# Kernel optimization log

Measured on AMD Instinct MI355X. Metric: run time of the kernel, lower is better.

## Reference

```python
import jax, jax.numpy as jnp
import numpy as np
import math


def _packet_loss_to_partial_patch(x, loss_rate):
    # Zero out randomly-chosen 1472-byte chunks of the NHWC-flattened tensor,
    # exactly mirroring the torch loop but as one vectorized masked multiply.
    B, C, H, W = x.shape
    xp = jnp.transpose(x, (0, 2, 3, 1)).reshape(-1)  # NHWC flatten
    n = xp.shape[0]
    elem_size = 4  # float32 bytes
    elems_per_chunk = 1472 // elem_size  # 368
    num_chunks = math.ceil(n * elem_size / 1472)
    num_lossy = int(math.ceil(num_chunks * (loss_rate / 100)))
    perm = jax.random.permutation(jax.random.key(1234), num_chunks)
    keep = jnp.ones((num_chunks,), xp.dtype).at[perm[:num_lossy]].set(0.0)
    elem_keep = jnp.repeat(keep, elems_per_chunk)[:n]
    xp = xp * elem_keep
    return jnp.transpose(xp.reshape(B, H, W, C), (0, 3, 1, 2))


def setup_inputs() -> dict:
    key = jax.random.key(0)
    ks = jax.random.split(key, 7)
    B, C, H, W = 32, 256, 56, 56
    r = 16
    s = 0.05
    return {
        "x": jax.random.normal(ks[0], (B, C, H, W), jnp.float32),
        "fc1_w": jax.random.normal(ks[1], (C // r, C), jnp.float32) * s,
        "fc2_w": jax.random.normal(ks[2], (C, C // r), jnp.float32) * s,
        "threshold": jnp.array([0.5], jnp.float32),
        "detect_w": jax.random.normal(ks[3], (C, C), jnp.float32) * s,
        "rec1_w": jax.random.normal(ks[4], (C, 2 * C), jnp.float32) * s,
        "rec2_w": jax.random.normal(ks[5], (C, C), jnp.float32) * s,
        "adapt_w": jax.random.normal(ks[6], (C, 1), jnp.float32) * s,
        "Packet_Loss_Rate": 50,
    }


def reference(x, fc1_w, fc2_w, threshold, detect_w, rec1_w, rec2_w, adapt_w, Packet_Loss_Rate):
    x = _packet_loss_to_partial_patch(x, Packet_Loss_Rate)
    B, C, H, W = x.shape
    # SE channel attention
    y = jnp.mean(x, axis=(2, 3))                              # [B, C]
    scores = jax.nn.sigmoid(jax.nn.relu(y @ fc1_w.T) @ fc2_w.T)  # [B, C]
    # packet-loss adaptation: Linear(1 -> C) applied to rate*ones([B,1])
    adapt = jnp.asarray(Packet_Loss_Rate, x.dtype) * adapt_w[:, 0]  # [C]
    mask = jax.nn.relu(scores + adapt[None, :] - threshold)   # [B, C]
    mask = mask[:, :, None, None]
    # 1x1 convs as channel GEMMs
    det = jnp.einsum('oc,bchw->bohw', detect_w, x)
    z = jnp.concatenate([x, jax.nn.sigmoid(det) * x], axis=1)  # [B, 2C, H, W]
    r = jax.nn.relu(jnp.einsum('oc,bchw->bohw', rec1_w, z))
    r = jnp.einsum('oc,bchw->bohw', rec2_w, r)
    return r * mask
```

## Files before the change

kernel.cpp:

```cpp
#include <hip/hip_runtime.h>
#include <stdint.h>

#define PARTITIONABLE 1

typedef float f32x4 __attribute__((ext_vector_type(4)));
typedef short bf16x8 __attribute__((ext_vector_type(8)));

namespace {
constexpr int Hh = 56, Ww = 56;
constexpr int HW = Hh * Ww;
constexpr int Bsz = 32, Cch = 256;
constexpr int NCH = 69811;
constexpr int HALF = 34906;
constexpr int NB2 = 4096;

constexpr int SC1_W   = 0;
constexpr int SC2_W   = 139648;
constexpr int BITS1_W = 279296;
constexpr int BITS2_W = 349120;
constexpr int R1_W    = 418944;
constexpr int R2_W    = 488768;
constexpr int HIST1_W = 558592;
constexpr int PRE1_W  = 562688;
constexpr int CNT1_W  = 566784;
constexpr int HIST2_W = 570880;
constexpr int PRE2_W  = 574976;
constexpr int CNT2_W  = 579072;
constexpr int Y_W     = 583168;

constexpr int KEEP_W  = 0;
constexpr int MASKV_W = 69824;
constexpr int WPACK_W = 78016;
}

__host__ __device__ constexpr uint32_t rotl32(uint32_t v, int r) {
  return (v << r) | (v >> (32 - r));
}
__host__ __device__ constexpr uint64_t tf2x32(uint32_t k0, uint32_t k1,
                                              uint32_t x0, uint32_t x1) {
  uint32_t ks2 = k0 ^ k1 ^ 0x1BD11BDAu;
  x0 += k0; x1 += k1;
  {const int R[4]={13,15,26,6};  for(int i=0;i<4;i++){x0+=x1;x1=rotl32(x1,R[i]);x1^=x0;}}
  x0 += k1;  x1 += ks2 + 1u;
  {const int R[4]={17,29,16,24}; for(int i=0;i<4;i++){x0+=x1;x1=rotl32(x1,R[i]);x1^=x0;}}
  x0 += ks2; x1 += k0 + 2u;
  {const int R[4]={13,15,26,6};  for(int i=0;i<4;i++){x0+=x1;x1=rotl32(x1,R[i]);x1^=x0;}}
  x0 += k0;  x1 += k1 + 3u;
  {const int R[4]={17,29,16,24}; for(int i=0;i<4;i++){x0+=x1;x1=rotl32(x1,R[i]);x1^=x0;}}
  x0 += k1;  x1 += ks2 + 4u;
  {const int R[4]={13,15,26,6};  for(int i=0;i<4;i++){x0+=x1;x1=rotl32(x1,R[i]);x1^=x0;}}
  x0 += ks2; x1 += k0 + 5u;
  return ((uint64_t)x0 << 32) | x1;
}

#if PARTITIONABLE
constexpr uint64_t KEY1 = tf2x32(0u, 1234u, 0u, 0u);
constexpr uint64_t SUB1 = tf2x32(0u, 1234u, 0u, 1u);
constexpr uint64_t SUB2 = tf2x32((uint32_t)(KEY1 >> 32), (uint32_t)KEY1, 0u, 1u);
constexpr uint32_t S1H = (uint32_t)(SUB1 >> 32), S1L = (uint32_t)SUB1;
constexpr uint32_t S2H = (uint32_t)(SUB2 >> 32), S2L = (uint32_t)SUB2;
#else
constexpr uint64_t E0 = tf2x32(0u, 1234u, 0u, 2u);
constexpr uint64_t E1 = tf2x32(0u, 1234u, 1u, 3u);
constexpr uint32_t K1H = (uint32_t)(E0 >> 32), K1L = (uint32_t)(E1 >> 32);
constexpr uint64_t F0 = tf2x32(K1H, K1L, 0u, 2u);
constexpr uint64_t F1 = tf2x32(K1H, K1L, 1u, 3u);
constexpr uint32_t S1H = (uint32_t)E0, S1L = (uint32_t)E1;
constexpr uint32_t S2H = (uint32_t)F0, S2L = (uint32_t)F1;
#endif

__device__ __forceinline__ uint32_t rnd_bits(uint32_t kh, uint32_t kl, uint32_t i) {
#if PARTITIONABLE
  uint64_t r = tf2x32(kh, kl, 0u, i);
  return (uint32_t)(r >> 32) ^ (uint32_t)r;
#else
  if (i < (uint32_t)HALF) {
    uint32_t x1 = (i + HALF < (uint32_t)NCH) ? i + HALF : 0u;
    return (uint32_t)(tf2x32(kh, kl, i, x1) >> 32);
  } else {
    return (uint32_t)tf2x32(kh, kl, i - HALF, i);
  }
#endif
}

__device__ __forceinline__ uint32_t f2bf(float f) {
  uint32_t u = __float_as_uint(f);
  return (u + 0x7FFFu + ((u >> 16) & 1u)) >> 16;
}
__device__ __forceinline__ float bf2f(uint32_t h) {
  return __uint_as_float(h << 16);
}

__global__ void k_bits(uint32_t* bits1, uint32_t* bits2,
                       uint32_t* hist1, uint32_t* hist2) {
  int i = blockIdx.x * 256 + threadIdx.x;
  if (i >= NCH) return;
  uint32_t b1 = rnd_bits(S1H, S1L, (uint32_t)i);
  uint32_t b2 = rnd_bits(S2H, S2L, (uint32_t)i);
  bits1[i] = b1; bits2[i] = b2;
  atomicAdd(&hist1[b1 >> 20], 1u);
  atomicAdd(&hist2[b2 >> 20], 1u);
}

__global__ __launch_bounds__(1024) void k_scan2(const uint32_t* h1, uint32_t* p1o,
                                                const uint32_t* h2, uint32_t* p2o) {
  const uint32_t* h = blockIdx.x ? h2 : h1;
  uint32_t* pre = blockIdx.x ? p2o : p1o;
  __shared__ uint32_t part[1024];
  int t = threadIdx.x;
  uint4 v = *(const uint4*)&h[t * 4];
  uint32_t s = v.x + v.y + v.z + v.w;
  part[t] = s;
  __syncthreads();
  for (int off = 1; off < 1024; off <<= 1) {
    uint32_t u = (t >= off) ? part[t - off] : 0u;
    __syncthreads();
    part[t] += u;
    __syncthreads();
  }
  uint32_t run = part[t] - s;
  uint4 o;
  o.x = run; o.y = run + v.x; o.z = o.y + v.y; o.w = o.z + v.z;
  *(uint4*)&pre[t * 4] = o;
}

__global__ void k_scatter2(const uint32_t* bits1, const uint32_t* pre1,
                           uint32_t* cnt1, uint64_t* sc1,
                           const uint32_t* bits2, const uint32_t* pre2,
                           uint32_t* cnt2, uint64_t* sc2) {
  int blk = blockIdx.x;
  bool second = blk >= 273;
  const uint32_t* bits = second ? bits2 : bits1;
  const uint32_t* pre  = second ? pre2  : pre1;
  uint32_t* cnt = second ? cnt2 : cnt1;
  uint64_t* sc  = second ? sc2  : sc1;
  int i = (second ? blk - 273 : blk) * 256 + threadIdx.x;
  if (i >= NCH) return;
  uint32_t b = bits[i], bk = b >> 20;
  uint32_t pos = pre[bk] + atomicAdd(&cnt[bk], 1u);
  sc[pos] = ((uint64_t)b << 32) | (uint32_t)i;
}

__global__ void k_rank2(const uint32_t* bits1, const uint32_t* pre1,
                        const uint32_t* hist1, const uint64_t* sc1, uint32_t* rk1,
                        const uint32_t* bits2, const uint32_t* pre2,
                        const uint32_t* hist2, const uint64_t* sc2, uint32_t* rk2) {
  int blk = blockIdx.x;
  bool second = blk >= 273;
  const uint32_t* bits = second ? bits2 : bits1;
  const uint32_t* pre  = second ? pre2  : pre1;
  const uint32_t* hist = second ? hist2 : hist1;
  const uint64_t* sc   = second ? sc2   : sc1;
  uint32_t* rnk = second ? rk2 : rk1;
  int i = (second ? blk - 273 : blk) * 256 + threadIdx.x;
  if (i >= NCH) return;
  uint32_t b = bits[i], bk = b >> 20;
  uint32_t s = pre[bk], n = hist[bk];
  uint64_t my = ((uint64_t)b << 32) | (uint32_t)i;
  uint32_t c = 0;
  for (uint32_t k = 0; k < n; ++k) c += (sc[s + k] < my) ? 1u : 0u;
  rnk[i] = s + c;
}

__global__ void k_keepwpack(const uint32_t* r1, const uint32_t* r2,
                            const int* plr, float* keep,
                            const float* __restrict__ dw,
                            const float* __restrict__ r1w,
                            const float* __restrict__ r2w,
                            ushort* __restrict__ wdp, ushort* __restrict__ w1p,
                            ushort* __restrict__ w2p) {
  int blk = blockIdx.x;
  if (blk < 273) {
    int j = blk * 256 + threadIdx.x;
    if (j >= NCH) return;
    int L = (NCH * plr[0] + 99) / 100;
    keep[j] = (r2[r1[j]] < (uint32_t)L) ? 0.f : 1.f;
    return;
  }
  int tid = (blk - 273) * 256 + threadIdx.x;
  const float* src;
  ushort* dst;
  if (tid < 8192) {
    int s = tid, ot = s >> 9, ks = (s >> 6) & 7, l = s & 63;
    src = dw + (ot * 16 + (l & 15)) * 256 + ks * 32 + (l >> 4) * 8;
    dst = wdp + s * 8;
  } else if (tid < 24576) {
    int s = tid - 8192, ot = s >> 10, ks = (s >> 6) & 15, l = s & 63;
    src = r1w + (ot * 16 + (l & 15)) * 512 + ks * 32 + (l >> 4) * 8;
    dst = w1p + s * 8;
  } else {
    int s = tid - 24576, ot = s >> 9, ks = (s >> 6) & 7, l = s & 63;
    src = r2w + (ot * 16 + (l & 15)) * 256 + ks * 32 + (l >> 4) * 8;
    dst = w2p + s * 8;
  }
  float4 v0 = *(const float4*)src;
  float4 v1 = *(const float4*)(src + 4);
  uint4 pk;
  pk.x = f2bf(v0.x) | (f2bf(v0.y) << 16);
  pk.y = f2bf(v0.z) | (f2bf(v0.w) << 16);
  pk.z = f2bf(v1.x) | (f2bf(v1.y) << 16);
  pk.w = f2bf(v1.z) | (f2bf(v1.w) << 16);
  *(uint4*)dst = pk;
}

__global__ void k_ymean(const float* __restrict__ x, const float* __restrict__ keep,
                        float* __restrict__ y) {
  int bc = blockIdx.x;
  int b = bc >> 8, c = bc & 255;
  const float4* row = (const float4*)(x + (size_t)bc * HW);
  int t = threadIdx.x;
  float s = 0.f;
  for (int q = t; q < HW / 4; q += 256) {
    float4 v = row[q];
    uint32_t base = (uint32_t)((b * HW + q * 4) * 256 + c);
    s += v.x * keep[base / 368u];
    s += v.y * keep[(base + 256u) / 368u];
    s += v.z * keep[(base + 512u) / 368u];
    s += v.w * keep[(base + 768u) / 368u];
  }
  for (int off = 32; off > 0; off >>= 1) s += __shfl_down(s, off);
  __shared__ float w4[4];
  if ((t & 63) == 0) w4[t >> 6] = s;
  __syncthreads();
  if (t == 0) y[bc] = (w4[0] + w4[1] + w4[2] + w4[3]) * (1.0f / HW);
}

__global__ void k_scores(const float* __restrict__ y, const float* __restrict__ fc1,
                         const float* __restrict__ fc2, const float* __restrict__ thr,
                         const float* __restrict__ aw, const int* __restrict__ plr,
                         float* __restrict__ maskv) {
  int b = blockIdx.x, t = threadIdx.x;
  __shared__ float ysh[256];
  __shared__ float hsh[16];
  ysh[t] = y[b * 256 + t];
  __syncthreads();
  if (t < 16) {
    float a = 0.f;
    for (int c = 0; c < 256; ++c) a += ysh[c] * fc1[t * 256 + c];
    hsh[t] = fmaxf(a, 0.f);
  }
  __syncthreads();
  float s = 0.f;
  #pragma unroll
  for (int j = 0; j < 16; ++j) s += hsh[j] * fc2[t * 16 + j];
  float sc = 1.f / (1.f + expf(-s));
  float m = sc + (float)plr[0] * aw[t] - thr[0];
  maskv[b * 256 + t] = fmaxf(m, 0.f);
}

__global__ __launch_bounds__(512, 4) void k_main(
    const float* __restrict__ x, const float* __restrict__ keep,
    const ushort* __restrict__ wdp, const ushort* __restrict__ w1p,
    const ushort* __restrict__ w2p, const float* __restrict__ maskv,
    float* __restrict__ out) {
  __shared__ __align__(16) short XT[16384];
  __shared__ __align__(16) short ST[16384];
  int tile = blockIdx.x;
  int bb = tile / 49, hw0 = (tile % 49) * 64;
  int t = threadIdx.x;
  int lane = t & 63, w = t >> 6;
  int l15 = lane & 15, lhi = lane >> 4;

  {
    const float* xb = x + (size_t)bb * (Cch * HW);
    uint32_t pixb = (uint32_t)(bb * HW + hw0);
    int p = lane;
    uint32_t ia0 = (pixb + (uint32_t)p) * 256u;
    uint32_t k0 = ia0 / 368u;
    uint32_t cstar = 368u * (k0 + 1u) - ia0;
    float kp0 = keep[k0];
    float kp1 = keep[k0 + 1];
    const float* xcol = xb + hw0 + p;
    int c0 = w * 32;
    #pragma unroll
    for (int k = 0; k < 4; ++k) {
      uint32_t pw0, pw1, pw2, pw3;
      #pragma unroll
      for (int h = 0; h < 4; ++h) {
        uint32_t ca = (uint32_t)(c0 + k * 8 + h * 2);
        float va = xcol[(size_t)ca * HW] * (ca < cstar ? kp0 : kp1);
        float vb = xcol[(size_t)(ca + 1u) * HW] * ((ca + 1u) < cstar ? kp0 : kp1);
        uint32_t pkv = f2bf(va) | (f2bf(vb) << 16);
        if (h == 0) pw0 = pkv; else if (h == 1) pw1 = pkv;
        else if (h == 2) pw2 = pkv; else pw3 = pkv;
      }
      uint4 pk; pk.x = pw0; pk.y = pw1; pk.z = pw2; pk.w = pw3;
      *(uint4*)&XT[(w * 4 + (p >> 4)) * 512 + ((p & 15) + 16 * k) * 8] = pk;
    }
  }
  __syncthreads();

  f32x4 zero4 = {0.f, 0.f, 0.f, 0.f};
  f32x4 acc[2][4];
  int row16a = (lhi >> 1);
  int sub4 = (lhi & 1) * 4;

  #pragma unroll
  for (int mt = 0; mt < 2; ++mt)
    #pragma unroll
    for (int nt = 0; nt < 4; ++nt) acc[mt][nt] = zero4;
  {
    const ushort* a0p = wdp + ((w * 2 + 0) * 8) * 512 + lane * 8;
    const ushort* a1p = wdp + ((w * 2 + 1) * 8) * 512 + lane * 8;
    bf16x8 a0 = *(const bf16x8*)a0p;
    bf16x8 a1 = *(const bf16x8*)a1p;
    #pragma unroll
    for (int ks = 0; ks < 8; ++ks) {
      bf16x8 na0 = a0, na1 = a1;
      if (ks < 7) {
        na0 = *(const bf16x8*)(a0p + (ks + 1) * 512);
        na1 = *(const bf16x8*)(a1p + (ks + 1) * 512);
      }
      #pragma unroll
      for (int nt = 0; nt < 4; ++nt) {
        bf16x8 b = *(const bf16x8*)&XT[(ks * 4 + nt) * 512 + lane * 8];
        acc[0][nt] = __builtin_amdgcn_mfma_f32_16x16x32_bf16(a0, b, acc[0][nt], 0, 0, 0);
        acc[1][nt] = __builtin_amdgcn_mfma_f32_16x16x32_bf16(a1, b, acc[1][nt], 0, 0, 0);
      }
      a0 = na0; a1 = na1;
    }
  }

  #pragma unroll
  for (int mt = 0; mt < 2; ++mt) {
    int row16 = mt * 2 + row16a;
    #pragma unroll
    for (int nt = 0; nt < 4; ++nt) {
      int off = (w * 4 + nt) * 512 + (l15 + 16 * row16) * 8 + sub4;
      ushort4 xv = *(const ushort4*)&XT[off];
      ushort4 sv;
      sv.x = (ushort)f2bf(bf2f(xv.x) / (1.f + __expf(-acc[mt][nt][0])));
      sv.y = (ushort)f2bf(bf2f(xv.y) / (1.f + __expf(-acc[mt][nt][1])));
      sv.z = (ushort)f2bf(bf2f(xv.z) / (1.f + __expf(-acc[mt][nt][2])));
      sv.w = (ushort)f2bf(bf2f(xv.w) / (1.f + __expf(-acc[mt][nt][3])));
      *(ushort4*)&ST[off] = sv;
    }
  }
  __syncthreads();

  f32x4 acc2[2][4];
  #pragma unroll
  for (int mt = 0; mt < 2; ++mt)
    #pragma unroll
    for (int nt = 0; nt < 4; ++nt) acc2[mt][nt] = zero4;
  {
    const ushort* a0p = w1p + ((w * 2 + 0) * 16) * 512 + lane * 8;
    const ushort* a1p = w1p + ((w * 2 + 1) * 16) * 512 + lane * 8;
    bf16x8 a0 = *(const bf16x8*)a0p;
    bf16x8 a1 = *(const bf16x8*)a1p;
    #pragma unroll
    for (int ks = 0; ks < 16; ++ks) {
      bf16x8 na0 = a0, na1 = a1;
      if (ks < 15) {
        na0 = *(const bf16x8*)(a0p + (ks + 1) * 512);
        na1 = *(const bf16x8*)(a1p + (ks + 1) * 512);
      }
      const short* bsrc = (ks < 8) ? &XT[(ks * 4) * 512] : &ST[((ks - 8) * 4) * 512];
      #pragma unroll
      for (int nt = 0; nt < 4; ++nt) {
        bf16x8 b = *(const bf16x8*)&bsrc[nt * 512 + lane * 8];
        acc2[0][nt] = __builtin_amdgcn_mfma_f32_16x16x32_bf16(a0, b, acc2[0][nt], 0, 0, 0);
        acc2[1][nt] = __builtin_amdgcn_mfma_f32_16x16x32_bf16(a1, b, acc2[1][nt], 0, 0, 0);
      }
      a0 = na0; a1 = na1;
    }
  }
  __syncthreads();

  #pragma unroll
  for (int mt = 0; mt < 2; ++mt) {
    int row16 = mt * 2 + row16a;
    #pragma unroll
    for (int nt = 0; nt < 4; ++nt) {
      int off = (w * 4 + nt) * 512 + (l15 + 16 * row16) * 8 + sub4;
      ushort4 rv;
      rv.x = (ushort)f2bf(fmaxf(acc2[mt][nt][0], 0.f));
      rv.y = (ushort)f2bf(fmaxf(acc2[mt][nt][1], 0.f));
      rv.z = (ushort)f2bf(fmaxf(acc2[mt][nt][2], 0.f));
      rv.w = (ushort)f2bf(fmaxf(acc2[mt][nt][3], 0.f));
      *(ushort4*)&XT[off] = rv;
    }
  }
  __syncthreads();

  #pragma unroll
  for (int mt = 0; mt < 2; ++mt)
    #pragma unroll
    for (int nt = 0; nt < 4; ++nt) acc[mt][nt] = zero4;
  {
    const ushort* a0p = w2p + ((w * 2 + 0) * 8) * 512 + lane * 8;
    const ushort* a1p = w2p + ((w * 2 + 1) * 8) * 512 + lane * 8;
    bf16x8 a0 = *(const bf16x8*)a0p;
    bf16x8 a1 = *(const bf16x8*)a1p;
    #pragma unroll
    for (int ks = 0; ks < 8; ++ks) {
      bf16x8 na0 = a0, na1 = a1;
      if (ks < 7) {
        na0 = *(const bf16x8*)(a0p + (ks + 1) * 512);
        na1 = *(const bf16x8*)(a1p + (ks + 1) * 512);
      }
      #pragma unroll
      for (int nt = 0; nt < 4; ++nt) {
        bf16x8 b = *(const bf16x8*)&XT[(ks * 4 + nt) * 512 + lane * 8];
        acc[0][nt] = __builtin_amdgcn_mfma_f32_16x16x32_bf16(a0, b, acc[0][nt], 0, 0, 0);
        acc[1][nt] = __builtin_amdgcn_mfma_f32_16x16x32_bf16(a1, b, acc[1][nt], 0, 0, 0);
      }
      a0 = na0; a1 = na1;
    }
  }

  #pragma unroll
  for (int mt = 0; mt < 2; ++mt)
    #pragma unroll
    for (int r = 0; r < 4; ++r) {
      int o = w * 32 + mt * 16 + 4 * lhi + r;
      float m = maskv[bb * 256 + o];
      float* orow = out + (size_t)(bb * 256 + o) * HW + hw0;
      #pragma unroll
      for (int nt = 0; nt < 4; ++nt)
        orow[nt * 16 + l15] = acc[mt][nt][r] * m;
    }
}

extern "C" void kernel_launch(void* const* d_in, const int* in_sizes, int n_in,
                              void* d_out, int out_size, void* d_ws, size_t ws_size,
                              hipStream_t stream) {
  const float* x   = (const float*)d_in[0];
  const float* fc1 = (const float*)d_in[1];
  const float* fc2 = (const float*)d_in[2];
  const float* thr = (const float*)d_in[3];
  const float* dw  = (const float*)d_in[4];
  const float* r1w = (const float*)d_in[5];
  const float* r2w = (const float*)d_in[6];
  const float* aw  = (const float*)d_in[7];
  const int*   plr = (const int*)d_in[8];

  float*    out = (float*)d_out;
  uint32_t* ob  = (uint32_t*)d_out;
  float*    ws  = (float*)d_ws;

  uint64_t* sc1   = (uint64_t*)(ob + SC1_W);
  uint64_t* sc2   = (uint64_t*)(ob + SC2_W);
  uint32_t* bits1 = ob + BITS1_W;
  uint32_t* bits2 = ob + BITS2_W;
  uint32_t* r1    = ob + R1_W;
  uint32_t* r2    = ob + R2_W;
  uint32_t* hist1 = ob + HIST1_W;
  uint32_t* pre1  = ob + PRE1_W;
  uint32_t* cnt1  = ob + CNT1_W;
  uint32_t* hist2 = ob + HIST2_W;
  uint32_t* pre2  = ob + PRE2_W;
  uint32_t* cnt2  = ob + CNT2_W;
  float*    yv    = (float*)(ob + Y_W);

  float*  keep  = ws + KEEP_W;
  float*  maskv = ws + MASKV_W;
  ushort* wdp   = (ushort*)(ws + WPACK_W);
  ushort* w1p   = wdp + 65536;
  ushort* w2p   = w1p + 131072;

  hipMemsetAsync((void*)(ob + HIST1_W), 0, (size_t)6 * NB2 * 4, stream);

  dim3 blk(256);
  k_bits<<<273, blk, 0, stream>>>(bits1, bits2, hist1, hist2);
  k_scan2<<<2, 1024, 0, stream>>>(hist1, pre1, hist2, pre2);
  k_scatter2<<<546, blk, 0, stream>>>(bits1, pre1, cnt1, sc1,
                                      bits2, pre2, cnt2, sc2);
  k_rank2<<<546, blk, 0, stream>>>(bits1, pre1, hist1, sc1, r1,
                                   bits2, pre2, hist2, sc2, r2);
  k_keepwpack<<<401, blk, 0, stream>>>(r1, r2, plr, keep, dw, r1w, r2w,
                                       wdp, w1p, w2p);
  k_ymean<<<8192, blk, 0, stream>>>(x, keep, yv);
  k_scores<<<32, blk, 0, stream>>>(yv, fc1, fc2, thr, aw, plr, maskv);
  k_main<<<1568, 512, 0, stream>>>(x, keep, wdp, w1p, w2p, maskv, out);
}
```

Baseline: 149.9 us.

## Split main kernel over 16 waves, use hardware bf16 pack, stage output in LDS

Measured after the change: 158.5 us. 5.8% more time.

```diff
diff --git a/kernel.cpp b/kernel.cpp
--- a/kernel.cpp
+++ b/kernel.cpp
@@ -89,6 +89,11 @@
 }
 __device__ __forceinline__ float bf2f(uint32_t h) {
   return __uint_as_float(h << 16);
+}
+__device__ __forceinline__ uint32_t cvtpk(float lo, float hi) {
+  uint32_t r;
+  asm("v_cvt_pk_bf16_f32 %0, %1, %2" : "=v"(r) : "v"(lo), "v"(hi));
+  return r;
 }
 
 __global__ void k_bits(uint32_t* bits1, uint32_t* bits2,
@@ -248,13 +253,12 @@
   maskv[b * 256 + t] = fmaxf(m, 0.f);
 }
 
-__global__ __launch_bounds__(512, 4) void k_main(
+__global__ __launch_bounds__(1024, 8) void k_main(
     const float* __restrict__ x, const float* __restrict__ keep,
     const ushort* __restrict__ wdp, const ushort* __restrict__ w1p,
     const ushort* __restrict__ w2p, const float* __restrict__ maskv,
     float* __restrict__ out) {
-  __shared__ __align__(16) short XT[16384];
-  __shared__ __align__(16) short ST[16384];
+  __shared__ __align__(16) short SM[32768];
   int tile = blockIdx.x;
   int bb = tile / 49, hw0 = (tile % 49) * 64;
   int t = threadIdx.x;
@@ -271,155 +275,138 @@
     float kp0 = keep[k0];
     float kp1 = keep[k0 + 1];
     const float* xcol = xb + hw0 + p;
-    int c0 = w * 32;
-    #pragma unroll
-    for (int k = 0; k < 4; ++k) {
-      uint32_t pw0, pw1, pw2, pw3;
+    int ks = w >> 1;
+    #pragma unroll
+    for (int k2 = 0; k2 < 2; ++k2) {
+      int k = (w & 1) * 2 + k2;
+      int cb = ks * 32 + k * 8;
+      uint32_t pw[4];
       #pragma unroll
       for (int h = 0; h < 4; ++h) {
-        uint32_t ca = (uint32_t)(c0 + k * 8 + h * 2);
+        uint32_t ca = (uint32_t)(cb + h * 2);
         float va = xcol[(size_t)ca * HW] * (ca < cstar ? kp0 : kp1);
         float vb = xcol[(size_t)(ca + 1u) * HW] * ((ca + 1u) < cstar ? kp0 : kp1);
-        uint32_t pkv = f2bf(va) | (f2bf(vb) << 16);
-        if (h == 0) pw0 = pkv; else if (h == 1) pw1 = pkv;
-        else if (h == 2) pw2 = pkv; else pw3 = pkv;
+        pw[h] = cvtpk(va, vb);
       }
-      uint4 pk; pk.x = pw0; pk.y = pw1; pk.z = pw2; pk.w = pw3;
-      *(uint4*)&XT[(w * 4 + (p >> 4)) * 512 + ((p & 15) + 16 * k) * 8] = pk;
+      uint4 pk; pk.x = pw[0]; pk.y = pw[1]; pk.z = pw[2]; pk.w = pw[3];
+      *(uint4*)&SM[(ks * 4 + (p >> 4)) * 512 + ((p & 15) + 16 * k) * 8] = pk;
     }
   }
   __syncthreads();
 
   f32x4 zero4 = {0.f, 0.f, 0.f, 0.f};
-  f32x4 acc[2][4];
-  int row16a = (lhi >> 1);
-  int sub4 = (lhi & 1) * 4;
-
-  #pragma unroll
-  for (int mt = 0; mt < 2; ++mt)
-    #pragma unroll
-    for (int nt = 0; nt < 4; ++nt) acc[mt][nt] = zero4;
-  {
-    const ushort* a0p = wdp + ((w * 2 + 0) * 8) * 512 + lane * 8;
-    const ushort* a1p = wdp + ((w * 2 + 1) * 8) * 512 + lane * 8;
-    bf16x8 a0 = *(const bf16x8*)a0p;
-    bf16x8 a1 = *(const bf16x8*)a1p;
+  f32x4 acc[4];
+  int stoff = ((w >> 1) * 4) * 512 +
+              (l15 + 16 * ((w & 1) * 2 + (lhi >> 1))) * 8 + (lhi & 1) * 4;
+
+  #pragma unroll
+  for (int nt = 0; nt < 4; ++nt) acc[nt] = zero4;
+  {
+    const ushort* ap = wdp + (w * 8) * 512 + lane * 8;
+    bf16x8 a0 = *(const bf16x8*)ap;
     #pragma unroll
     for (int ks = 0; ks < 8; ++ks) {
-      bf16x8 na0 = a0, na1 = a1;
-      if (ks < 7) {
-        na0 = *(const bf16x8*)(a0p + (ks + 1) * 512);
-        na1 = *(const bf16x8*)(a1p + (ks + 1) * 512);
-      }
+      bf16x8 na0 = a0;
+      if (ks < 7) na0 = *(const bf16x8*)(ap + (ks + 1) * 512);
       #pragma unroll
       for (int nt = 0; nt < 4; ++nt) {
-        bf16x8 b = *(const bf16x8*)&XT[(ks * 4 + nt) * 512 + lane * 8];
-        acc[0][nt] = __builtin_amdgcn_mfma_f32_16x16x32_bf16(a0, b, acc[0][nt], 0, 0, 0);
-        acc[1][nt] = __builtin_amdgcn_mfma_f32_16x16x32_bf16(a1, b, acc[1][nt], 0, 0, 0);
+        bf16x8 b = *(const bf16x8*)&SM[(ks * 4 + nt) * 512 + lane * 8];
+        acc[nt] = __builtin_amdgcn_mfma_f32_16x16x32_bf16(a0, b, acc[nt], 0, 0, 0);
       }
-      a0 = na0; a1 = na1;
-    }
-  }
-
-  #pragma unroll
-  for (int mt = 0; mt < 2; ++mt) {
-    int row16 = mt * 2 + row16a;
-    #pragma unroll
-    for (int nt = 0; nt < 4; ++nt) {
-      int off = (w * 4 + nt) * 512 + (l15 + 16 * row16) * 8 + sub4;
-      ushort4 xv = *(const ushort4*)&XT[off];
-      ushort4 sv;
-      sv.x = (ushort)f2bf(bf2f(xv.x) / (1.f + __expf(-acc[mt][nt][0])));
-      sv.y = (ushort)f2bf(bf2f(xv.y) / (1.f + __expf(-acc[mt][nt][1])));
-      sv.z = (ushort)f2bf(bf2f(xv.z) / (1.f + __expf(-acc[mt][nt][2])));
-      sv.w = (ushort)f2bf(bf2f(xv.w) / (1.f + __expf(-acc[mt][nt][3])));
-      *(ushort4*)&ST[off] = sv;
-    }
-  }
-  __syncthreads();
-
-  f32x4 acc2[2][4];
-  #pragma unroll
-  for (int mt = 0; mt < 2; ++mt)
-    #pragma unroll
-    for (int nt = 0; nt < 4; ++nt) acc2[mt][nt] = zero4;
-  {
-    const ushort* a0p = w1p + ((w * 2 + 0) * 16) * 512 + lane * 8;
-    const ushort* a1p = w1p + ((w * 2 + 1) * 16) * 512 + lane * 8;
-    bf16x8 a0 = *(const bf16x8*)a0p;
-    bf16x8 a1 = *(const bf16x8*)a1p;
+      a0 = na0;
+    }
+  }
+
+  #pragma unroll
+  for (int nt = 0; nt < 4; ++nt) {
+    int off = stoff + nt * 512;
+    ushort4 xv = *(const ushort4*)&SM[off];
+    float s0 = bf2f(xv.x) / (1.f + __expf(-acc[nt][0]));
+    float s1 = bf2f(xv.y) / (1.f + __expf(-acc[nt][1]));
+    float s2 = bf2f(xv.z) / (1.f + __expf(-acc[nt][2]));
+    float s3 = bf2f(xv.w) / (1.f + __expf(-acc[nt][3]));
+    uint2 sv;
+    sv.x = cvtpk(s0, s1);
+    sv.y = cvtpk(s2, s3);
+    *(uint2*)&SM[16384 + off] = sv;
+  }
+  __syncthreads();
+
+  f32x4 acc2[4];
+  #pragma unroll
+  for (int nt = 0; nt < 4; ++nt) acc2[nt] = zero4;
+  {
+    const ushort* ap = w1p + (w * 16) * 512 + lane * 8;
+    bf16x8 a0 = *(const bf16x8*)ap;
     #pragma unroll
     for (int ks = 0; ks < 16; ++ks) {
-      bf16x8 na0 = a0, na1 = a1;
-      if (ks < 15) {
-        na0 = *(const bf16x8*)(a0p + (ks + 1) * 512);
-        na1 = *(const bf16x8*)(a1p + (ks + 1) * 512);
-      }
-      const short* bsrc = (ks < 8) ? &XT[(ks * 4) * 512] : &ST[((ks - 8) * 4) * 512];
+      bf16x8 na0 = a0;
+      if (ks < 15) na0 = *(const bf16x8*)(ap + (ks + 1) * 512);
       #pragma unroll
       for (int nt = 0; nt < 4; ++nt) {
-        bf16x8 b = *(const bf16x8*)&bsrc[nt * 512 + lane * 8];
-        acc2[0][nt] = __builtin_amdgcn_mfma_f32_16x16x32_bf16(a0, b, acc2[0][nt], 0, 0, 0);
-        acc2[1][nt] = __builtin_amdgcn_mfma_f32_16x16x32_bf16(a1, b, acc2[1][nt], 0, 0, 0);
+        bf16x8 b = *(const bf16x8*)&SM[(ks * 4 + nt) * 512 + lane * 8];
+        acc2[nt] = __builtin_amdgcn_mfma_f32_16x16x32_bf16(a0, b, acc2[nt], 0, 0, 0);
       }
-      a0 = na0; a1 = na1;
-    }
-  }
-  __syncthreads();
-
-  #pragma unroll
-  for (int mt = 0; mt < 2; ++mt) {
-    int row16 = mt * 2 + row16a;
-    #pragma unroll
-    for (int nt = 0; nt < 4; ++nt) {
-      int off = (w * 4 + nt) * 512 + (l15 + 16 * row16) * 8 + sub4;
-      ushort4 rv;
-      rv.x = (ushort)f2bf(fmaxf(acc2[mt][nt][0], 0.f));
-      rv.y = (ushort)f2bf(fmaxf(acc2[mt][nt][1], 0.f));
-      rv.z = (ushort)f2bf(fmaxf(acc2[mt][nt][2], 0.f));
-      rv.w = (ushort)f2bf(fmaxf(acc2[mt][nt][3], 0.f));
-      *(ushort4*)&XT[off] = rv;
-    }
-  }
-  __syncthreads();
-
-  #pragma unroll
-  for (int mt = 0; mt < 2; ++mt)
-    #pragma unroll
-    for (int nt = 0; nt < 4; ++nt) acc[mt][nt] = zero4;
-  {
-    const ushort* a0p = w2p + ((w * 2 + 0) * 8) * 512 + lane * 8;
-    const ushort* a1p = w2p + ((w * 2 + 1) * 8) * 512 + lane * 8;
-    bf16x8 a0 = *(const bf16x8*)a0p;
-    bf16x8 a1 = *(const bf16x8*)a1p;
+      a0 = na0;
+    }
+  }
+  __syncthreads();
+
+  #pragma unroll
+  for (int nt = 0; nt < 4; ++nt) {
+    int off = stoff + nt * 512;
+    uint2 rv;
+    rv.x = cvtpk(fmaxf(acc2[nt][0], 0.f), fmaxf(acc2[nt][1], 0.f));
+    rv.y = cvtpk(fmaxf(acc2[nt][2], 0.f), fmaxf(acc2[nt][3], 0.f));
+    *(uint2*)&SM[off] = rv;
+  }
+  __syncthreads();
+
+  #pragma unroll
+  for (int nt = 0; nt < 4; ++nt) acc[nt] = zero4;
+  {
+    const ushort* ap = w2p + (w * 8) * 512 + lane * 8;
+    bf16x8 a0 = *(const bf16x8*)ap;
     #pragma unroll
     for (int ks = 0; ks < 8; ++ks) {
-      bf16x8 na0 = a0, na1 = a1;
-      if (ks < 7) {
-        na0 = *(const bf16x8*)(a0p + (ks + 1) * 512);
-        na1 = *(const bf16x8*)(a1p + (ks + 1) * 512);
-      }
+      bf16x8 na0 = a0;
+      if (ks < 7) na0 = *(const bf16x8*)(ap + (ks + 1) * 512);
       #pragma unroll
       for (int nt = 0; nt < 4; ++nt) {
-        bf16x8 b = *(const bf16x8*)&XT[(ks * 4 + nt) * 512 + lane * 8];
-        acc[0][nt] = __builtin_amdgcn_mfma_f32_16x16x32_bf16(a0, b, acc[0][nt], 0, 0, 0);
-        acc[1][nt] = __builtin_amdgcn_mfma_f32_16x16x32_bf16(a1, b, acc[1][nt], 0, 0, 0);
+        bf16x8 b = *(const bf16x8*)&SM[(ks * 4 + nt) * 512 + lane * 8];
+        acc[nt] = __builtin_amdgcn_mfma_f32_16x16x32_bf16(a0, b, acc[nt], 0, 0, 0);
       }
-      a0 = na0; a1 = na1;
-    }
-  }
-
-  #pragma unroll
-  for (int mt = 0; mt < 2; ++mt)
+      a0 = na0;
+    }
+  }
+  __syncthreads();
+
+  {
+    float* EP = (float*)SM;
+    int sw = ((lhi & 1) << 2) | ((lhi >> 1) << 4);
     #pragma unroll
     for (int r = 0; r < 4; ++r) {
-      int o = w * 32 + mt * 16 + 4 * lhi + r;
-      float m = maskv[bb * 256 + o];
-      float* orow = out + (size_t)(bb * 256 + o) * HW + hw0;
+      int c = w * 16 + 4 * lhi + r;
+      float m = maskv[bb * 256 + c];
       #pragma unroll
       for (int nt = 0; nt < 4; ++nt)
-        orow[nt * 16 + l15] = acc[mt][nt][r] * m;
-    }
+        EP[c * 64 + ((nt * 16 + l15) ^ sw)] = acc[nt][r] * m;
+    }
+  }
+  __syncthreads();
+  {
+    const float* EP = (const float*)SM;
+    float* op = out + (size_t)bb * (Cch * HW) + hw0;
+    #pragma unroll
+    for (int q = 0; q < 4; ++q) {
+      int idx4 = q * 1024 + t;
+      int c = idx4 >> 4;
+      int colw = (idx4 & 15) * 4;
+      int p = colw ^ ((((c >> 2) & 1) << 2) | (((c >> 3) & 1) << 4));
+      f32x4 v = *(const f32x4*)&EP[idx4 * 4];
+      *(f32x4*)(op + (size_t)c * HW + p) = v;
+    }
+  }
 }
 
 extern "C" void kernel_launch(void* const* d_in, const int* in_sizes, int n_in,
@@ -472,5 +459,5 @@
                                        wdp, w1p, w2p);
   k_ymean<<<8192, blk, 0, stream>>>(x, keep, yv);
   k_scores<<<32, blk, 0, stream>>>(yv, fc1, fc2, thr, aw, plr, maskv);
-  k_main<<<1568, 512, 0, stream>>>(x, keep, wdp, w1p, w2p, maskv, out);
-}
+  k_main<<<1568, 1024, 0, stream>>>(x, keep, wdp, w1p, w2p, maskv, out);
+}
```

## Retile k_main warps to 4x2 MFMA tiles, fuse ymean+scores, use packed bf16 cvt

Applied to the files above, without the earlier changes.

Measured after the change: 230.1 us. 53.6% more time.

```diff
diff --git a/kernel.cpp b/kernel.cpp
--- a/kernel.cpp
+++ b/kernel.cpp
@@ -26,7 +26,8 @@
 constexpr int HIST2_W = 570880;
 constexpr int PRE2_W  = 574976;
 constexpr int CNT2_W  = 579072;
-constexpr int Y_W     = 583168;
+constexpr int DONE_W  = 583168;
+constexpr int Y_W     = 583200;
 
 constexpr int KEEP_W  = 0;
 constexpr int MASKV_W = 69824;
@@ -89,6 +90,11 @@
 }
 __device__ __forceinline__ float bf2f(uint32_t h) {
   return __uint_as_float(h << 16);
+}
+__device__ __forceinline__ uint32_t cvtpk(float lo, float hi) {
+  uint32_t r;
+  asm("v_cvt_pk_bf16_f32 %0, %1, %2" : "=v"(r) : "v"(lo), "v"(hi));
+  return r;
 }
 
 __global__ void k_bits(uint32_t* bits1, uint32_t* bits2,
@@ -203,36 +209,45 @@
   *(uint4*)dst = pk;
 }
 
-__global__ void k_ymean(const float* __restrict__ x, const float* __restrict__ keep,
-                        float* __restrict__ y) {
-  int bc = blockIdx.x;
-  int b = bc >> 8, c = bc & 255;
-  const float4* row = (const float4*)(x + (size_t)bc * HW);
-  int t = threadIdx.x;
-  float s = 0.f;
-  for (int q = t; q < HW / 4; q += 256) {
-    float4 v = row[q];
-    uint32_t base = (uint32_t)((b * HW + q * 4) * 256 + c);
-    s += v.x * keep[base / 368u];
-    s += v.y * keep[(base + 256u) / 368u];
-    s += v.z * keep[(base + 512u) / 368u];
-    s += v.w * keep[(base + 768u) / 368u];
-  }
-  for (int off = 32; off > 0; off >>= 1) s += __shfl_down(s, off);
-  __shared__ float w4[4];
-  if ((t & 63) == 0) w4[t >> 6] = s;
-  __syncthreads();
-  if (t == 0) y[bc] = (w4[0] + w4[1] + w4[2] + w4[3]) * (1.0f / HW);
-}
-
-__global__ void k_scores(const float* __restrict__ y, const float* __restrict__ fc1,
-                         const float* __restrict__ fc2, const float* __restrict__ thr,
-                         const float* __restrict__ aw, const int* __restrict__ plr,
-                         float* __restrict__ maskv) {
-  int b = blockIdx.x, t = threadIdx.x;
+__global__ __launch_bounds__(256) void k_ymean2(
+    const float* __restrict__ x, const float* __restrict__ keep,
+    float* __restrict__ y, uint32_t* __restrict__ done,
+    const float* __restrict__ fc1, const float* __restrict__ fc2,
+    const float* __restrict__ thr, const float* __restrict__ aw,
+    const int* __restrict__ plr, float* __restrict__ maskv) {
+  int blk = blockIdx.x;
+  int b = blk >> 5, sub = blk & 31;
+  int t = threadIdx.x, lane = t & 63, v = t >> 6;
+  #pragma unroll
+  for (int cc = 0; cc < 2; ++cc) {
+    int c = sub * 8 + v * 2 + cc;
+    int row = b * 256 + c;
+    const float4* rowp = (const float4*)(x + (size_t)row * HW);
+    float s = 0.f;
+    for (int q = lane; q < HW / 4; q += 64) {
+      float4 vv = rowp[q];
+      uint32_t base = (uint32_t)((b * HW + q * 4) * 256 + c);
+      s += vv.x * keep[base / 368u];
+      s += vv.y * keep[(base + 256u) / 368u];
+      s += vv.z * keep[(base + 512u) / 368u];
+      s += vv.w * keep[(base + 768u) / 368u];
+    }
+    for (int off = 32; off > 0; off >>= 1) s += __shfl_down(s, off);
+    if (lane == 0) y[row] = s * (1.0f / HW);
+  }
+  __threadfence();
+  __syncthreads();
+  __shared__ int lastf;
+  if (t == 0) {
+    uint32_t ret = atomicAdd(&done[b], 1u);
+    lastf = (ret == 31u) ? 1 : 0;
+  }
+  __syncthreads();
+  if (!lastf) return;
+  __threadfence();
   __shared__ float ysh[256];
   __shared__ float hsh[16];
-  ysh[t] = y[b * 256 + t];
+  ysh[t] = ((volatile const float*)y)[b * 256 + t];
   __syncthreads();
   if (t < 16) {
     float a = 0.f;
@@ -260,6 +275,7 @@
   int t = threadIdx.x;
   int lane = t & 63, w = t >> 6;
   int l15 = lane & 15, lhi = lane >> 4;
+  int g = w >> 1, h = w & 1;
 
   {
     const float* xb = x + (size_t)bb * (Cch * HW);
@@ -276,13 +292,13 @@
     for (int k = 0; k < 4; ++k) {
       uint32_t pw0, pw1, pw2, pw3;
       #pragma unroll
-      for (int h = 0; h < 4; ++h) {
-        uint32_t ca = (uint32_t)(c0 + k * 8 + h * 2);
+      for (int hh = 0; hh < 4; ++hh) {
+        uint32_t ca = (uint32_t)(c0 + k * 8 + hh * 2);
         float va = xcol[(size_t)ca * HW] * (ca < cstar ? kp0 : kp1);
         float vb = xcol[(size_t)(ca + 1u) * HW] * ((ca + 1u) < cstar ? kp0 : kp1);
-        uint32_t pkv = f2bf(va) | (f2bf(vb) << 16);
-        if (h == 0) pw0 = pkv; else if (h == 1) pw1 = pkv;
-        else if (h == 2) pw2 = pkv; else pw3 = pkv;
+        uint32_t pkv = cvtpk(va, vb);
+        if (hh == 0) pw0 = pkv; else if (hh == 1) pw1 = pkv;
+        else if (hh == 2) pw2 = pkv; else pw3 = pkv;
       }
       uint4 pk; pk.x = pw0; pk.y = pw1; pk.z = pw2; pk.w = pw3;
       *(uint4*)&XT[(w * 4 + (p >> 4)) * 512 + ((p & 15) + 16 * k) * 8] = pk;
@@ -291,134 +307,138 @@
   __syncthreads();
 
   f32x4 zero4 = {0.f, 0.f, 0.f, 0.f};
-  f32x4 acc[2][4];
+  f32x4 acc[4][2];
   int row16a = (lhi >> 1);
   int sub4 = (lhi & 1) * 4;
 
   #pragma unroll
-  for (int mt = 0; mt < 2; ++mt)
-    #pragma unroll
-    for (int nt = 0; nt < 4; ++nt) acc[mt][nt] = zero4;
+  for (int mt = 0; mt < 4; ++mt)
+    #pragma unroll
+    for (int n2 = 0; n2 < 2; ++n2) acc[mt][n2] = zero4;
   {
-    const ushort* a0p = wdp + ((w * 2 + 0) * 8) * 512 + lane * 8;
-    const ushort* a1p = wdp + ((w * 2 + 1) * 8) * 512 + lane * 8;
-    bf16x8 a0 = *(const bf16x8*)a0p;
-    bf16x8 a1 = *(const bf16x8*)a1p;
+    const ushort* ap = wdp + (size_t)(g * 32) * 512 + lane * 8;
+    bf16x8 a[4], na[4];
+    #pragma unroll
+    for (int mt = 0; mt < 4; ++mt) a[mt] = *(const bf16x8*)(ap + (size_t)mt * 8 * 512);
     #pragma unroll
     for (int ks = 0; ks < 8; ++ks) {
-      bf16x8 na0 = a0, na1 = a1;
-      if (ks < 7) {
-        na0 = *(const bf16x8*)(a0p + (ks + 1) * 512);
-        na1 = *(const bf16x8*)(a1p + (ks + 1) * 512);
+      #pragma unroll
+      for (int mt = 0; mt < 4; ++mt)
+        na[mt] = (ks < 7) ? *(const bf16x8*)(ap + (size_t)(mt * 8 + ks + 1) * 512) : a[mt];
+      #pragma unroll
+      for (int n2 = 0; n2 < 2; ++n2) {
+        bf16x8 b = *(const bf16x8*)&XT[(ks * 4 + 2 * h + n2) * 512 + lane * 8];
+        #pragma unroll
+        for (int mt = 0; mt < 4; ++mt)
+          acc[mt][n2] = __builtin_amdgcn_mfma_f32_16x16x32_bf16(a[mt], b, acc[mt][n2], 0, 0, 0);
       }
       #pragma unroll
-      for (int nt = 0; nt < 4; ++nt) {
-        bf16x8 b = *(const bf16x8*)&XT[(ks * 4 + nt) * 512 + lane * 8];
-        acc[0][nt] = __builtin_amdgcn_mfma_f32_16x16x32_bf16(a0, b, acc[0][nt], 0, 0, 0);
-        acc[1][nt] = __builtin_amdgcn_mfma_f32_16x16x32_bf16(a1, b, acc[1][nt], 0, 0, 0);
+      for (int mt = 0; mt < 4; ++mt) a[mt] = na[mt];
+    }
+  }
+
+  #pragma unroll
+  for (int mt = 0; mt < 4; ++mt) {
+    int cg32 = 2 * g + (mt >> 1);
+    int row16 = (mt & 1) * 2 + row16a;
+    #pragma unroll
+    for (int n2 = 0; n2 < 2; ++n2) {
+      int nt = 2 * h + n2;
+      int off = (cg32 * 4 + nt) * 512 + (l15 + 16 * row16) * 8 + sub4;
+      ushort4 xv = *(const ushort4*)&XT[off];
+      float s0 = bf2f(xv.x) / (1.f + __expf(-acc[mt][n2][0]));
+      float s1 = bf2f(xv.y) / (1.f + __expf(-acc[mt][n2][1]));
+      float s2 = bf2f(xv.z) / (1.f + __expf(-acc[mt][n2][2]));
+      float s3 = bf2f(xv.w) / (1.f + __expf(-acc[mt][n2][3]));
+      uint2 sv;
+      sv.x = cvtpk(s0, s1);
+      sv.y = cvtpk(s2, s3);
+      *(uint2*)&ST[off] = sv;
+    }
+  }
+  __syncthreads();
+
+  f32x4 acc2[4][2];
+  #pragma unroll
+  for (int mt = 0; mt < 4; ++mt)
+    #pragma unroll
+    for (int n2 = 0; n2 < 2; ++n2) acc2[mt][n2] = zero4;
+  {
+    const ushort* ap = w1p + (size_t)(g * 64) * 512 + lane * 8;
+    bf16x8 a[4], na[4];
+    #pragma unroll
+    for (int mt = 0; mt < 4; ++mt) a[mt] = *(const bf16x8*)(ap + (size_t)mt * 16 * 512);
+    #pragma unroll
+    for (int ks = 0; ks < 16; ++ks) {
+      #pragma unroll
+      for (int mt = 0; mt < 4; ++mt)
+        na[mt] = (ks < 15) ? *(const bf16x8*)(ap + (size_t)(mt * 16 + ks + 1) * 512) : a[mt];
+      const short* bsrc = (ks < 8) ? &XT[(ks * 4) * 512] : &ST[((ks - 8) * 4) * 512];
+      #pragma unroll
+      for (int n2 = 0; n2 < 2; ++n2) {
+        bf16x8 b = *(const bf16x8*)&bsrc[(2 * h + n2) * 512 + lane * 8];
+        #pragma unroll
+        for (int mt = 0; mt < 4; ++mt)
+          acc2[mt][n2] = __builtin_amdgcn_mfma_f32_16x16x32_bf16(a[mt], b, acc2[mt][n2], 0, 0, 0);
       }
-      a0 = na0; a1 = na1;
-    }
-  }
-
-  #pragma unroll
-  for (int mt = 0; mt < 2; ++mt) {
-    int row16 = mt * 2 + row16a;
-    #pragma unroll
-    for (int nt = 0; nt < 4; ++nt) {
-      int off = (w * 4 + nt) * 512 + (l15 + 16 * row16) * 8 + sub4;
-      ushort4 xv = *(const ushort4*)&XT[off];
-      ushort4 sv;
-      sv.x = (ushort)f2bf(bf2f(xv.x) / (1.f + __expf(-acc[mt][nt][0])));
-      sv.y = (ushort)f2bf(bf2f(xv.y) / (1.f + __expf(-acc[mt][nt][1])));
-      sv.z = (ushort)f2bf(bf2f(xv.z) / (1.f + __expf(-acc[mt][nt][2])));
-      sv.w = (ushort)f2bf(bf2f(xv.w) / (1.f + __expf(-acc[mt][nt][3])));
-      *(ushort4*)&ST[off] = sv;
-    }
-  }
-  __syncthreads();
-
-  f32x4 acc2[2][4];
-  #pragma unroll
-  for (int mt = 0; mt < 2; ++mt)
-    #pragma unroll
-    for (int nt = 0; nt < 4; ++nt) acc2[mt][nt] = zero4;
+      #pragma unroll
+      for (int mt = 0; mt < 4; ++mt) a[mt] = na[mt];
+    }
+  }
+  __syncthreads();
+
+  #pragma unroll
+  for (int mt = 0; mt < 4; ++mt) {
+    int cg32 = 2 * g + (mt >> 1);
+    int row16 = (mt & 1) * 2 + row16a;
+    #pragma unroll
+    for (int n2 = 0; n2 < 2; ++n2) {
+      int nt = 2 * h + n2;
+      int off = (cg32 * 4 + nt) * 512 + (l15 + 16 * row16) * 8 + sub4;
+      uint2 rv;
+      rv.x = cvtpk(fmaxf(acc2[mt][n2][0], 0.f), fmaxf(acc2[mt][n2][1], 0.f));
+      rv.y = cvtpk(fmaxf(acc2[mt][n2][2], 0.f), fmaxf(acc2[mt][n2][3], 0.f));
+      *(uint2*)&XT[off] = rv;
+    }
+  }
+  __syncthreads();
+
+  #pragma unroll
+  for (int mt = 0; mt < 4; ++mt)
+    #pragma unroll
+    for (int n2 = 0; n2 < 2; ++n2) acc[mt][n2] = zero4;
   {
-    const ushort* a0p = w1p + ((w * 2 + 0) * 16) * 512 + lane * 8;
-    const ushort* a1p = w1p + ((w * 2 + 1) * 16) * 512 + lane * 8;
-    bf16x8 a0 = *(const bf16x8*)a0p;
-    bf16x8 a1 = *(const bf16x8*)a1p;
-    #pragma unroll
-    for (int ks = 0; ks < 16; ++ks) {
-      bf16x8 na0 = a0, na1 = a1;
-      if (ks < 15) {
-        na0 = *(const bf16x8*)(a0p + (ks + 1) * 512);
-        na1 = *(const bf16x8*)(a1p + (ks + 1) * 512);
+    const ushort* ap = w2p + (size_t)(g * 32) * 512 + lane * 8;
+    bf16x8 a[4], na[4];
+    #pragma unroll
+    for (int mt = 0; mt < 4; ++mt) a[mt] = *(const bf16x8*)(ap + (size_t)mt * 8 * 512);
+    #pragma unroll
+    for (int ks = 0; ks < 8; ++ks) {
+      #pragma unroll
+      for (int mt = 0; mt < 4; ++mt)
+        na[mt] = (ks < 7) ? *(const bf16x8*)(ap + (size_t)(mt * 8 + ks + 1) * 512) : a[mt];
+      #pragma unroll
+      for (int n2 = 0; n2 < 2; ++n2) {
+        bf16x8 b = *(const bf16x8*)&XT[(ks * 4 + 2 * h + n2) * 512 + lane * 8];
+        #pragma unroll
+        for (int mt = 0; mt < 4; ++mt)
+          acc[mt][n2] = __builtin_amdgcn_mfma_f32_16x16x32_bf16(a[mt], b, acc[mt][n2], 0, 0, 0);
       }
-      const short* bsrc = (ks < 8) ? &XT[(ks * 4) * 512] : &ST[((ks - 8) * 4) * 512];
-      #pragma unroll
-      for (int nt = 0; nt < 4; ++nt) {
-        bf16x8 b = *(const bf16x8*)&bsrc[nt * 512 + lane * 8];
-        acc2[0][nt] = __builtin_amdgcn_mfma_f32_16x16x32_bf16(a0, b, acc2[0][nt], 0, 0, 0);
-        acc2[1][nt] = __builtin_amdgcn_mfma_f32_16x16x32_bf16(a1, b, acc2[1][nt], 0, 0, 0);
-      }
-      a0 = na0; a1 = na1;
-    }
-  }
-  __syncthreads();
-
-  #pragma unroll
-  for (int mt = 0; mt < 2; ++mt) {
-    int row16 = mt * 2 + row16a;
-    #pragma unroll
-    for (int nt = 0; nt < 4; ++nt) {
-      int off = (w * 4 + nt) * 512 + (l15 + 16 * row16) * 8 + sub4;
-      ushort4 rv;
-      rv.x = (ushort)f2bf(fmaxf(acc2[mt][nt][0], 0.f));
-      rv.y = (ushort)f2bf(fmaxf(acc2[mt][nt][1], 0.f));
-      rv.z = (ushort)f2bf(fmaxf(acc2[mt][nt][2], 0.f));
-      rv.w = (ushort)f2bf(fmaxf(acc2[mt][nt][3], 0.f));
-      *(ushort4*)&XT[off] = rv;
-    }
-  }
-  __syncthreads();
-
-  #pragma unroll
-  for (int mt = 0; mt < 2; ++mt)
-    #pragma unroll
-    for (int nt = 0; nt < 4; ++nt) acc[mt][nt] = zero4;
-  {
-    const ushort* a0p = w2p + ((w * 2 + 0) * 8) * 512 + lane * 8;
-    const ushort* a1p = w2p + ((w * 2 + 1) * 8) * 512 + lane * 8;
-    bf16x8 a0 = *(const bf16x8*)a0p;
-    bf16x8 a1 = *(const bf16x8*)a1p;
-    #pragma unroll
-    for (int ks = 0; ks < 8; ++ks) {
-      bf16x8 na0 = a0, na1 = a1;
-      if (ks < 7) {
-        na0 = *(const bf16x8*)(a0p + (ks + 1) * 512);
-        na1 = *(const bf16x8*)(a1p + (ks + 1) * 512);
-      }
-      #pragma unroll
-      for (int nt = 0; nt < 4; ++nt) {
-        bf16x8 b = *(const bf16x8*)&XT[(ks * 4 + nt) * 512 + lane * 8];
-        acc[0][nt] = __builtin_amdgcn_mfma_f32_16x16x32_bf16(a0, b, acc[0][nt], 0, 0, 0);
-        acc[1][nt] = __builtin_amdgcn_mfma_f32_16x16x32_bf16(a1, b, acc[1][nt], 0, 0, 0);
-      }
-      a0 = na0; a1 = na1;
-    }
-  }
-
-  #pragma unroll
-  for (int mt = 0; mt < 2; ++mt)
+      #pragma unroll
+      for (int mt = 0; mt < 4; ++mt) a[mt] = na[mt];
+    }
+  }
+
+  #pragma unroll
+  for (int mt = 0; mt < 4; ++mt)
     #pragma unroll
     for (int r = 0; r < 4; ++r) {
-      int o = w * 32 + mt * 16 + 4 * lhi + r;
+      int o = g * 64 + mt * 16 + 4 * lhi + r;
       float m = maskv[bb * 256 + o];
       float* orow = out + (size_t)(bb * 256 + o) * HW + hw0;
       #pragma unroll
-      for (int nt = 0; nt < 4; ++nt)
-        orow[nt * 16 + l15] = acc[mt][nt][r] * m;
+      for (int n2 = 0; n2 < 2; ++n2)
+        orow[(2 * h + n2) * 16 + l15] = acc[mt][n2][r] * m;
     }
 }
 
@@ -443,14 +463,15 @@
   uint64_t* sc2   = (uint64_t*)(ob + SC2_W);
   uint32_t* bits1 = ob + BITS1_W;
   uint32_t* bits2 = ob + BITS2_W;
-  uint32_t* r1    = ob + R1_W;
-  uint32_t* r2    = ob + R2_W;
+  uint32_t* rk1   = ob + R1_W;
+  uint32_t* rk2   = ob + R2_W;
   uint32_t* hist1 = ob + HIST1_W;
   uint32_t* pre1  = ob + PRE1_W;
   uint32_t* cnt1  = ob + CNT1_W;
   uint32_t* hist2 = ob + HIST2_W;
   uint32_t* pre2  = ob + PRE2_W;
   uint32_t* cnt2  = ob + CNT2_W;
+  uint32_t* done  = ob + DONE_W;
   float*    yv    = (float*)(ob + Y_W);
 
   float*  keep  = ws + KEEP_W;
@@ -459,18 +480,18 @@
   ushort* w1p   = wdp + 65536;
   ushort* w2p   = w1p + 131072;
 
-  hipMemsetAsync((void*)(ob + HIST1_W), 0, (size_t)6 * NB2 * 4, stream);
+  hipMemsetAsync((void*)(ob + HIST1_W), 0, (size_t)6 * NB2 * 4 + 128, stream);
 
   dim3 blk(256);
   k_bits<<<273, blk, 0, stream>>>(bits1, bits2, hist1, hist2);
   k_scan2<<<2, 1024, 0, stream>>>(hist1, pre1, hist2, pre2);
   k_scatter2<<<546, blk, 0, stream>>>(bits1, pre1, cnt1, sc1,
                                       bits2, pre2, cnt2, sc2);
-  k_rank2<<<546, blk, 0, stream>>>(bits1, pre1, hist1, sc1, r1,
-                                   bits2, pre2, hist2, sc2, r2);
-  k_keepwpack<<<401, blk, 0, stream>>>(r1, r2, plr, keep, dw, r1w, r2w,
+  k_rank2<<<546, blk, 0, stream>>>(bits1, pre1, hist1, sc1, rk1,
+                                   bits2, pre2, hist2, sc2, rk2);
+  k_keepwpack<<<401, blk, 0, stream>>>(rk1, rk2, plr, keep, dw, r1w, r2w,
                                        wdp, w1p, w2p);
-  k_ymean<<<8192, blk, 0, stream>>>(x, keep, yv);
-  k_scores<<<32, blk, 0, stream>>>(yv, fc1, fc2, thr, aw, plr, maskv);
+  k_ymean2<<<1024, blk, 0, stream>>>(x, keep, yv, done, fc1, fc2, thr, aw,
+                                     plr, maskv);
   k_main<<<1568, 512, 0, stream>>>(x, keep, wdp, w1p, w2p, maskv, out);
 }
```
